# Kernel optimization log

Measured on AMD Instinct MI355X. Metric: run time of the kernel, lower is better.

The kernel has to match this reference:

```python
import jax, jax.numpy as jnp
import numpy as np

N, E = 20000, 640000
LATENT, HID, OUT, HEADS = 512, 256, 128, 2
NEG_SLOPE = 0.2


def setup_inputs() -> dict:
    key = jax.random.key(0)
    ks = jax.random.split(key, 12)
    s = 0.02
    return {
        "z": jax.random.normal(ks[0], (N, LATENT), dtype=jnp.float32),
        "edge_index": jax.random.randint(ks[1], (2, E), 0, N, dtype=jnp.int64),
        "W1": jax.random.normal(ks[2], (LATENT, HID), dtype=jnp.float32) * s,
        "b1": jnp.zeros((HID,), dtype=jnp.float32),
        "W2": jax.random.normal(ks[3], (HID, HID * HEADS), dtype=jnp.float32) * s,
        "b2": jnp.zeros((HID * HEADS,), dtype=jnp.float32),
        "Wg": jax.random.normal(ks[4], (HID * HEADS, HEADS * OUT), dtype=jnp.float32) * s,
        "att_src": jax.random.normal(ks[5], (HEADS, OUT), dtype=jnp.float32) * s,
        "att_dst": jax.random.normal(ks[6], (HEADS, OUT), dtype=jnp.float32) * s,
        "bias_g": jnp.zeros((HEADS * OUT,), dtype=jnp.float32),
        "W3": jax.random.normal(ks[7], (OUT * HEADS, 512), dtype=jnp.float32) * s,
        "b3": jnp.zeros((512,), dtype=jnp.float32),
    }


def _gat_conv(x, edge_index, Wg, att_src, att_dst, bias_g):
    n = x.shape[0]
    # add self loops (PyG GATConv default add_self_loops=True)
    loops = jnp.tile(jnp.arange(n, dtype=edge_index.dtype)[None, :], (2, 1))
    ei = jnp.concatenate([edge_index, loops], axis=1)
    src, dst = ei[0], ei[1]
    xp = (x @ Wg).reshape(n, HEADS, OUT)          # [N,H,C]
    a_src = jnp.einsum('nhc,hc->nh', xp, att_src)  # [N,H]
    a_dst = jnp.einsum('nhc,hc->nh', xp, att_dst)
    alpha = jax.nn.leaky_relu(a_src[src] + a_dst[dst], NEG_SLOPE)  # [E+N,H]
    amax = jax.ops.segment_max(alpha, dst, num_segments=n)
    alpha = jnp.exp(alpha - amax[dst])
    denom = jax.ops.segment_sum(alpha, dst, num_segments=n)
    alpha = alpha / jnp.maximum(denom[dst], 1e-16)
    msg = xp[src] * alpha[:, :, None]              # [E+N,H,C]
    out = jax.ops.segment_sum(msg, dst, num_segments=n)  # [N,H,C]
    return out.reshape(n, HEADS * OUT) + bias_g


def reference(z, edge_index, W1, b1, W2, b2, Wg, att_src, att_dst, bias_g, W3, b3):
    x = jax.nn.relu(z @ W1 + b1)
    x = jax.nn.relu(x @ W2 + b2)
    x = _gat_conv(x, edge_index, Wg, att_src, att_dst, bias_g)
    return x @ W3 + b3
```

## Files before the change

### kernel.cpp

```cpp
#include <hip/hip_runtime.h>
#include <hip/hip_bf16.h>
#include <float.h>

#define N_NODES 20000
#define LATENT  512
#define HID     256
#define OUT_C   128
#define HEADS   2
#define HC      256
#define NEG_SLOPE 0.2f

typedef _Float16 half8 __attribute__((ext_vector_type(8)));
typedef __attribute__((ext_vector_type(4))) float f32x4;
typedef __attribute__((ext_vector_type(2))) float f32x2;

__device__ __forceinline__ ushort f2h(float v) {
    _Float16 h = (_Float16)v;
    return *(ushort*)&h;
}
__device__ __forceinline__ float h2f(ushort u) {
    _Float16 h = *(_Float16*)&u;
    return (float)h;
}

#if __has_builtin(__builtin_amdgcn_cvt_pk_fp8_f32) && __has_builtin(__builtin_amdgcn_cvt_pk_f32_fp8)
#define FP8_HW 1
#else
#define FP8_HW 0
#endif

__device__ __forceinline__ uint f32_to_e4m3(float v) {
#if FP8_HW
    return (uint)(__builtin_amdgcn_cvt_pk_fp8_f32(v, v, 0, false) & 0xff);
#else
    _Float16 hf = (_Float16)(v * 0.00390625f);
    uint hb = *(ushort*)&hf;
    uint s = (hb >> 8) & 0x80;
    uint mag = hb & 0x7fff;
    mag = (mag + 0x3f + ((mag >> 7) & 1)) >> 7;
    if (mag > 0x7e) mag = 0x7e;
    return s | mag;
#endif
}

__device__ __forceinline__ void gl_lds16(const ushort* g, ushort* l) {
    __builtin_amdgcn_global_load_lds(
        (const __attribute__((address_space(1))) unsigned int*)g,
        (__attribute__((address_space(3))) unsigned int*)l, 16, 0, 0);
}

template<int BN, int LOGNBY>
__global__ __launch_bounds__(256, 4) void gemm_f16(
    const ushort* __restrict__ A, const ushort* __restrict__ BT,
    const float* __restrict__ bias,
    float* __restrict__ Cf, ushort* __restrict__ Ch,
    unsigned char* __restrict__ C8,
    const float* __restrict__ attS, const float* __restrict__ attD,
    float* __restrict__ aS, float* __restrict__ aD,
    int M, int N, int K, int relu)
{
    static_assert(BN == 64, "vmcnt immediates assume 3 DMAs/chunk");
    constexpr int NI  = BN / 32;
    constexpr int BUF = 4096 + BN * 32;
    __shared__ ushort lds[3 * BUF];

    const int t = threadIdx.x;
    const int l = t & 63;
    const int w = t >> 6;
    const int wm = (w >> 1) * 64;
    const int wn = (w & 1) * (BN / 2);
    const int lm = l & 15;
    const int q  = l >> 4;
    const int q4 = q * 4;

    const int T  = (int)gridDim.x;
    const int qq = T >> 3, rr = T & 7;
    const int kx = (int)blockIdx.x & 7;
    const int jx = (int)blockIdx.x >> 3;
    const int lin = kx * qq + (kx < rr ? kx : rr) + jx;
    const int row0 = (lin >> LOGNBY) * 128;
    const int col0 = (lin & ((1 << LOGNBY) - 1)) * BN;

    const int jr0 = w * 16 + (l >> 2);
    const int gsh = (((l & 3) ^ ((l >> 4) & 3)) << 3);
    const ushort* gA0 = A + (size_t)(row0 + jr0) * K + gsh;
    const ushort* gA1 = gA0 + (size_t)64 * K;
    const ushort* gB0 = BT + (size_t)(col0 + jr0) * K + gsh;
    const int dA0 = w * 512, dA1 = (4 + w) * 512;
    const int dB0 = 4096 + w * 512;

    const int csw = ((q ^ ((lm >> 2) & 3)) << 3);

    const f32x4 zf = {0.f, 0.f, 0.f, 0.f};
    f32x4 acc[4][NI];
    #pragma unroll
    for (int i = 0; i < 4; ++i)
        #pragma unroll
        for (int j = 0; j < NI; ++j) acc[i][j] = zf;

    const int NC = K >> 5;

    auto issue = [&](int c) {
        ushort* B = lds + (size_t)(c % 3) * BUF;
        const int kk = c * 32;
        gl_lds16(gA0 + kk, B + dA0);
        gl_lds16(gA1 + kk, B + dA1);
        gl_lds16(gB0 + kk, B + dB0);
    };

    auto compute = [&](int c) {
        const ushort* B = lds + (size_t)(c % 3) * BUF;
        half8 bf[NI];
        #pragma unroll
        for (int ni = 0; ni < NI; ++ni) {
            const int boff = (wn + ni * 16 + lm) * 32 + csw;
            bf[ni] = *(const half8*)&B[4096 + boff];
        }
        #pragma unroll
        for (int mi = 0; mi < 4; ++mi) {
            const int aoff = (wm + mi * 16 + lm) * 32 + csw;
            half8 af = *(const half8*)&B[aoff];
            #pragma unroll
            for (int ni = 0; ni < NI; ++ni)
                acc[mi][ni] = __builtin_amdgcn_mfma_f32_16x16x32_f16(
                    af, bf[ni], acc[mi][ni], 0, 0, 0);
        }
    };

    issue(0); issue(1);
    for (int c = 0; c < NC; ++c) {
        __builtin_amdgcn_sched_barrier(0);
        if (c + 1 < NC) asm volatile("s_waitcnt vmcnt(3)" ::: "memory");
        else            asm volatile("s_waitcnt vmcnt(0)" ::: "memory");
        __builtin_amdgcn_s_barrier();
        __builtin_amdgcn_sched_barrier(0);
        if (c + 2 < NC) issue(c + 2);
        compute(c);
    }

    #pragma unroll
    for (int mi = 0; mi < 4; ++mi) {
        #pragma unroll
        for (int ni = 0; ni < NI; ++ni) {
            const int col = col0 + wn + ni * 16 + lm;
            const float bv = bias ? bias[col] : 0.f;
            #pragma unroll
            for (int r = 0; r < 4; ++r) {
                const int row = row0 + wm + mi * 16 + q4 + r;
                if (row >= M) continue;
                float v = acc[mi][ni][r] + bv;
                if (relu) v = fmaxf(v, 0.f);
                const size_t idx = (size_t)row * N + col;
                if (Cf) Cf[idx] = v;
                if (Ch) Ch[idx] = f2h(v);
                if (C8) C8[idx] = (unsigned char)f32_to_e4m3(v);
            }
        }
    }

    if (aS) {
        const int h = (col0 >= OUT_C) ? 1 : 0;
        float asv[NI], adv[NI];
        #pragma unroll
        for (int ni = 0; ni < NI; ++ni) {
            const int c = col0 + wn + ni * 16 + lm;
            asv[ni] = attS[c];
            adv[ni] = attD[c];
        }
        #pragma unroll
        for (int mi = 0; mi < 4; ++mi) {
            #pragma unroll
            for (int r = 0; r < 4; ++r) {
                const int row = row0 + wm + mi * 16 + q4 + r;
                float ps = 0.f, pd = 0.f;
                #pragma unroll
                for (int ni = 0; ni < NI; ++ni) {
                    ps += acc[mi][ni][r] * asv[ni];
                    pd += acc[mi][ni][r] * adv[ni];
                }
                #pragma unroll
                for (int off = 8; off > 0; off >>= 1) {
                    ps += __shfl_xor(ps, off);
                    pd += __shfl_xor(pd, off);
                }
                if (lm == 0 && row < M) {
                    atomicAdd(&aS[2 * row + h], ps);
                    atomicAdd(&aD[2 * row + h], pd);
                }
            }
        }
    }
}

#define CVT_BLOCKS 10000
#define TR_BLOCKS  2048
__global__ __launch_bounds__(256) void prologue_kernel(
    const float* __restrict__ z, ushort* __restrict__ z_f16,
    int* deg, int* cursor, float* aS, float* aD, int n,
    const float* __restrict__ W1, const float* __restrict__ W2,
    const float* __restrict__ Wg, const float* __restrict__ W3,
    ushort* __restrict__ T1, ushort* __restrict__ T2,
    ushort* __restrict__ Tg, ushort* __restrict__ T3)
{
    const int b = blockIdx.x;
    if (b < CVT_BLOCKS) {
        int i = b * 256 + threadIdx.x;
        if (i < n) {
            deg[i] = 0; cursor[i] = 0;
            ((float2*)aS)[i] = make_float2(0.f, 0.f);
            ((float2*)aD)[i] = make_float2(0.f, 0.f);
        }
        float4 v = ((const float4*)z)[i];
        ((ushort4*)z_f16)[i] = make_ushort4(f2h(v.x), f2h(v.y), f2h(v.z), f2h(v.w));
    } else {
        int idx = (b - CVT_BLOCKS) * 256 + threadIdx.x;
        int which = idx >> 17, i = idx & 131071;
        const float* W; ushort* T; int K, N;
        if (which == 0)      { W = W1; T = T1; K = 512; N = 256; }
        else if (which == 1) { W = W2; T = T2; K = 256; N = 512; }
        else if (which == 2) { W = Wg; T = Tg; K = 512; N = 256; }
        else                 { W = W3; T = T3; K = 256; N = 512; }
        int k = i / N, nn = i - k * N;
        T[(size_t)nn * K + k] = f2h(W[i]);
    }
}

__global__ __launch_bounds__(256) void hist_kernel(
    const int* __restrict__ dst, int* deg, int E_real, int ET)
{
    int e = blockIdx.x * blockDim.x + threadIdx.x;
    if (e >= ET) return;
    int d = (e < E_real) ? dst[e] : (e - E_real);
    atomicAdd(&deg[d], 1);
}

__global__ __launch_bounds__(1024) void scan_kernel(
    const int* __restrict__ deg, int* __restrict__ rowptr, int n)
{
    __shared__ int part[1024];
    const int t = threadIdx.x;
    const int chunk = (n + 1023) / 1024;
    const int lo = t * chunk;
    const int hi = min(lo + chunk, n);
    int s = 0;
    for (int i = lo; i < hi; ++i) s += deg[i];
    part[t] = s;
    __syncthreads();
    #pragma unroll
    for (int off = 1; off < 1024; off <<= 1) {
        int add = (t >= off) ? part[t - off] : 0;
        __syncthreads();
        part[t] += add;
        __syncthreads();
    }
    int run = part[t] - s;
    for (int i = lo; i < hi; ++i) { rowptr[i] = run; run += deg[i]; }
    if (t == 1023) rowptr[n] = part[1023];
}

__global__ __launch_bounds__(256) void scatter_kernel(
    const int* __restrict__ src, const int* __restrict__ dst,
    const int* __restrict__ rowptr, int* cursor,
    int* __restrict__ sorted_src, int E_real, int ET)
{
    int e = blockIdx.x * blockDim.x + threadIdx.x;
    if (e >= ET) return;
    int s, d;
    if (e < E_real) { s = src[e]; d = dst[e]; }
    else            { s = e - E_real; d = s; }
    int pos = rowptr[d] + atomicAdd(&cursor[d], 1);
    sorted_src[pos] = s;
}

__global__ __launch_bounds__(256) void gat_aggregate(
    const int* __restrict__ rowptr, const int* __restrict__ sorted_src,
    const float* __restrict__ a_src, const float* __restrict__ a_dst,
    const unsigned char* __restrict__ xp8, const float* __restrict__ bias_g,
    ushort* __restrict__ xg, int n)
{
    const int d = blockIdx.x * 4 + (threadIdx.x >> 6);
    if (d >= n) return;
    const int lane = threadIdx.x & 63;
    const int hsel = lane & 32;
    const int start = rowptr[d], end = rowptr[d + 1];

    const float ad0 = a_dst[2 * d + 0];
    const float ad1 = a_dst[2 * d + 1];

    float4 acc = make_float4(0.f, 0.f, 0.f, 0.f);
    float denom = 0.f;

    for (int e0 = start; e0 < end; e0 += 32) {
        const int cnt = min(32, end - e0);
        const int idx = lane & 31;
        float wsel = 0.f; int off = 0;
        if (idx < cnt) {
            int s = sorted_src[e0 + idx];
            float v0 = a_src[2 * s + 0] + ad0;
            float v1 = a_src[2 * s + 1] + ad1;
            v0 = (v0 > 0.f) ? v0 : NEG_SLOPE * v0;
            v1 = (v1 > 0.f) ? v1 : NEG_SLOPE * v1;
            wsel = (lane < 32) ? __expf(v0) : __expf(v1);
            off = s * HC;
        }
        int j = 0;
        for (; j + 8 <= cnt; j += 8) {
            float w_[8]; int o_[8];
            #pragma unroll
            for (int u = 0; u < 8; ++u) {
                w_[u] = __shfl(wsel, (j + u) + hsel);
                o_[u] = __shfl(off, j + u);
            }
            uint v_[8];
            #pragma unroll
            for (int u = 0; u < 8; ++u)
                v_[u] = *(const uint*)(xp8 + o_[u] + 4 * lane);
            #pragma unroll
            for (int u = 0; u < 8; ++u) {
                denom += w_[u];
#if FP8_HW
                f32x2 lo = __builtin_amdgcn_cvt_pk_f32_fp8((int)v_[u], false);
                f32x2 hi = __builtin_amdgcn_cvt_pk_f32_fp8((int)v_[u], true);
                acc.x += w_[u] * lo.x; acc.y += w_[u] * lo.y;
                acc.z += w_[u] * hi.x; acc.w += w_[u] * hi.y;
#else
                const float wu = w_[u] * 256.0f;
                const uint b = v_[u];
                acc.x += wu * h2f(((b & 0x80u) << 8) | ((b & 0x7fu) << 7));
                acc.y += wu * h2f((((b >> 8) & 0x80u) << 8) | (((b >> 8) & 0x7fu) << 7));
                acc.z += wu * h2f((((b >> 16) & 0x80u) << 8) | (((b >> 16) & 0x7fu) << 7));
                acc.w += wu * h2f((((b >> 24) & 0x80u) << 8) | (((b >> 24) & 0x7fu) << 7));
#endif
            }
        }
        for (; j < cnt; ++j) {
            const float w = __shfl(wsel, j + hsel);
            const int   o = __shfl(off, j);
            const uint  b = *(const uint*)(xp8 + o + 4 * lane);
            denom += w;
#if FP8_HW
            f32x2 lo = __builtin_amdgcn_cvt_pk_f32_fp8((int)b, false);
            f32x2 hi = __builtin_amdgcn_cvt_pk_f32_fp8((int)b, true);
            acc.x += w * lo.x; acc.y += w * lo.y;
            acc.z += w * hi.x; acc.w += w * hi.y;
#else
            const float wu = w * 256.0f;
            acc.x += wu * h2f(((b & 0x80u) << 8) | ((b & 0x7fu) << 7));
            acc.y += wu * h2f((((b >> 8) & 0x80u) << 8) | (((b >> 8) & 0x7fu) << 7));
            acc.z += wu * h2f((((b >> 16) & 0x80u) << 8) | (((b >> 16) & 0x7fu) << 7));
            acc.w += wu * h2f((((b >> 24) & 0x80u) << 8) | (((b >> 24) & 0x7fu) << 7));
#endif
        }
    }

    const float inv = 1.f / fmaxf(denom, 1e-16f);
    const int c = 4 * lane;
    const float4 bg = *(const float4*)(bias_g + c);
    const size_t base = ((size_t)d * HC + c) >> 2;
    ((ushort4*)xg)[base] = make_ushort4(
        f2h(acc.x * inv + bg.x), f2h(acc.y * inv + bg.y),
        f2h(acc.z * inv + bg.z), f2h(acc.w * inv + bg.w));
}

extern "C" void kernel_launch(void* const* d_in, const int* in_sizes, int n_in,
                              void* d_out, int out_size, void* d_ws, size_t ws_size,
                              hipStream_t stream)
{
    const float* z       = (const float*)d_in[0];
    const int*   ei      = (const int*)d_in[1];
    const float* W1      = (const float*)d_in[2];
    const float* b1      = (const float*)d_in[3];
    const float* W2      = (const float*)d_in[4];
    const float* b2      = (const float*)d_in[5];
    const float* Wg      = (const float*)d_in[6];
    const float* att_src = (const float*)d_in[7];
    const float* att_dst = (const float*)d_in[8];
    const float* bias_g  = (const float*)d_in[9];
    const float* W3      = (const float*)d_in[10];
    const float* b3      = (const float*)d_in[11];
    float* out = (float*)d_out;

    const int n = N_NODES;
    const int E_real = in_sizes[1] / 2;
    const int ET = E_real + n;
    const int* src = ei;
    const int* dst = ei + E_real;

    char* p = (char*)d_ws;
    auto alloc = [&](size_t bytes) {
        char* r = p;
        p += (bytes + 63) & ~(size_t)63;
        return r;
    };
    const int np = n + 128;
    ushort* z_f16  = (ushort*)alloc((size_t)np * LATENT * 2);
    ushort* x1_f16 = (ushort*)alloc((size_t)np * HID * 2);
    unsigned char* xp8 = (unsigned char*)alloc((size_t)n * HC);
    ushort* W1T = (ushort*)alloc((size_t)LATENT * HID * 2);
    ushort* W2T = (ushort*)alloc((size_t)HID * 512 * 2);
    ushort* WgT = (ushort*)alloc((size_t)512 * HC * 2);
    ushort* W3T = (ushort*)alloc((size_t)HC * 512 * 2);
    float* a_src = (float*)alloc((size_t)2 * n * 4);
    float* a_dst = (float*)alloc((size_t)2 * n * 4);
    int* deg        = (int*)alloc((size_t)n * 4);
    int* rowptr     = (int*)alloc(((size_t)n + 1) * 4);
    int* cursor     = (int*)alloc((size_t)n * 4);
    int* sorted_src = (int*)alloc((size_t)ET * 4);
    ushort* x2_f16 = z_f16;
    ushort* xg_f16 = x1_f16;

    const int gm128 = (n + 127) / 128;

    prologue_kernel<<<CVT_BLOCKS + TR_BLOCKS, 256, 0, stream>>>(
        z, z_f16, deg, cursor, a_src, a_dst, n,
        W1, W2, Wg, W3, W1T, W2T, WgT, W3T);
    hist_kernel<<<(ET + 255) / 256, 256, 0, stream>>>(dst, deg, E_real, ET);
    scan_kernel<<<1, 1024, 0, stream>>>(deg, rowptr, n);
    scatter_kernel<<<(ET + 255) / 256, 256, 0, stream>>>(
        src, dst, rowptr, cursor, sorted_src, E_real, ET);

    gemm_f16<64, 2><<<gm128 * 4, 256, 0, stream>>>(
        z_f16, W1T, b1, nullptr, x1_f16, nullptr,
        nullptr, nullptr, nullptr, nullptr, n, HID, LATENT, 1);
    gemm_f16<64, 3><<<gm128 * 8, 256, 0, stream>>>(
        x1_f16, W2T, b2, nullptr, x2_f16, nullptr,
        nullptr, nullptr, nullptr, nullptr, n, 512, HID, 1);
    gemm_f16<64, 2><<<gm128 * 4, 256, 0, stream>>>(
        x2_f16, WgT, nullptr, nullptr, nullptr, xp8,
        att_src, att_dst, a_src, a_dst, n, HC, 512, 0);

    gat_aggregate<<<(n + 3) / 4, 256, 0, stream>>>(
        rowptr, sorted_src, a_src, a_dst, xp8, bias_g, xg_f16, n);

    gemm_f16<64, 3><<<gm128 * 8, 256, 0, stream>>>(
        xg_f16, W3T, b3, out, nullptr, nullptr,
        nullptr, nullptr, nullptr, nullptr, n, 512, HC, 0);
}
```

Baseline: 314.9 us.

## Fuse three MLP GEMMs into one kernel keeping intermediates in LDS

Replaces the three separate GEMM launches (W1, W2, Wg with attention-score epilogue) with a single 512-thread kernel. Each block handles 64 rows and keeps the x1 and x2 intermediates in LDS as swizzled f16, streaming weight chunks through a three-stage global-to-LDS buffer. This removes the HBM round trips for x1 and x2 and two launches. In exchange each block uses 128KB of LDS, so occupancy is one block per CU, and every block re-reads the full weight matrices.

New measurement: 296.5 us. 5.8% less time.

```diff
diff --git a/kernel.cpp b/kernel.cpp
--- a/kernel.cpp
+++ b/kernel.cpp
@@ -49,14 +49,217 @@
         (__attribute__((address_space(3))) unsigned int*)l, 16, 0, 0);
 }
 
+__global__ __launch_bounds__(512) void fused_mlp(
+    const ushort* __restrict__ z16, const ushort* __restrict__ W1T,
+    const float* __restrict__ b1, const ushort* __restrict__ W2T,
+    const float* __restrict__ b2, const ushort* __restrict__ WgT,
+    const float* __restrict__ attS, const float* __restrict__ attD,
+    float* __restrict__ aS, float* __restrict__ aD,
+    unsigned char* __restrict__ xp8, int M)
+{
+    __shared__ ushort lds[65536];
+
+    const int t = threadIdx.x;
+    const int l = t & 63;
+    const int w = t >> 6;
+    const int wr = w & 3;
+    const int wc = w >> 2;
+    const int lm = l & 15;
+    const int q  = l >> 4;
+    const int q4 = q * 4;
+    const int row0 = (int)blockIdx.x * 64;
+    const int lr16 = l >> 2;
+    const int gsh = (((l & 3) ^ ((l >> 4) & 3)) << 3);
+    const int csw = ((q ^ ((lm >> 2) & 3)) << 3);
+
+    constexpr int X1 = 0;
+    constexpr int X2 = 16384;
+    constexpr int SB = 49152;
+
+    auto p1b = [&](int c) { int b = c % 3; return b == 0 ? SB : b == 1 ? X2 : X2 + 10240; };
+    auto p2b = [&](int c) { int b = c % 3; return b == 0 ? SB : b == 1 ? X2 : X2 + 16384; };
+    auto p3b = [&](int c) { int b = c % 3; return b == 0 ? SB : b == 1 ? SB + 8192 : X1; };
+
+    auto issue1 = [&](int c) {
+        ushort* B = &lds[p1b(c)];
+        const int kk = c * 32;
+        #pragma unroll
+        for (int u = 0; u < 3; ++u) {
+            const int ii = w + u * 8;
+            if (ii < 20) {
+                const ushort* g = (ii < 4)
+                    ? z16 + (size_t)(row0 + ii * 16 + lr16) * 512 + kk + gsh
+                    : W1T + (size_t)((ii - 4) * 16 + lr16) * 512 + kk + gsh;
+                gl_lds16(g, B + ii * 512);
+            }
+        }
+    };
+    auto issue2 = [&](int c) {
+        ushort* B = &lds[p2b(c)];
+        const int kk = c * 32;
+        #pragma unroll
+        for (int u = 0; u < 4; ++u) {
+            const int ii = w + u * 8;
+            gl_lds16(W2T + (size_t)(ii * 16 + lr16) * 256 + kk + gsh, B + ii * 512);
+        }
+    };
+    auto issue3 = [&](int c) {
+        ushort* B = &lds[p3b(c)];
+        const int kk = c * 32;
+        #pragma unroll
+        for (int u = 0; u < 2; ++u) {
+            const int ii = w + u * 8;
+            gl_lds16(WgT + (size_t)(ii * 16 + lr16) * 512 + kk + gsh, B + ii * 512);
+        }
+    };
+
+    auto wait3i = [&](int c, int NC) {
+        __builtin_amdgcn_sched_barrier(0);
+        if (c + 1 < NC) {
+            if (w < 4) asm volatile("s_waitcnt vmcnt(3)" ::: "memory");
+            else       asm volatile("s_waitcnt vmcnt(2)" ::: "memory");
+        } else         asm volatile("s_waitcnt vmcnt(0)" ::: "memory");
+        __builtin_amdgcn_s_barrier();
+        __builtin_amdgcn_sched_barrier(0);
+    };
+    auto wait4 = [&](int c, int NC) {
+        __builtin_amdgcn_sched_barrier(0);
+        if (c + 1 < NC) asm volatile("s_waitcnt vmcnt(4)" ::: "memory");
+        else            asm volatile("s_waitcnt vmcnt(0)" ::: "memory");
+        __builtin_amdgcn_s_barrier();
+        __builtin_amdgcn_sched_barrier(0);
+    };
+    auto wait2 = [&](int c, int NC) {
+        __builtin_amdgcn_sched_barrier(0);
+        if (c + 1 < NC) asm volatile("s_waitcnt vmcnt(2)" ::: "memory");
+        else            asm volatile("s_waitcnt vmcnt(0)" ::: "memory");
+        __builtin_amdgcn_s_barrier();
+        __builtin_amdgcn_sched_barrier(0);
+    };
+
+    const f32x4 zf = {0.f, 0.f, 0.f, 0.f};
+
+    f32x4 acc1[8];
+    #pragma unroll
+    for (int i = 0; i < 8; ++i) acc1[i] = zf;
+
+    issue1(0); issue1(1);
+    for (int c = 0; c < 16; ++c) {
+        wait3i(c, 16);
+        if (c + 2 < 16) issue1(c + 2);
+        const ushort* B = &lds[p1b(c)];
+        half8 af = *(const half8*)&B[(wr * 16 + lm) * 32 + csw];
+        #pragma unroll
+        for (int ni = 0; ni < 8; ++ni) {
+            half8 bf = *(const half8*)&B[2048 + (wc * 128 + ni * 16 + lm) * 32 + csw];
+            acc1[ni] = __builtin_amdgcn_mfma_f32_16x16x32_f16(af, bf, acc1[ni], 0, 0, 0);
+        }
+    }
+    __builtin_amdgcn_s_barrier();
+    issue2(0); issue2(1);
+    #pragma unroll
+    for (int ni = 0; ni < 8; ++ni) {
+        const int col = wc * 128 + ni * 16 + lm;
+        const float bv = b1[col];
+        const int ch = col >> 5, c5 = col & 31;
+        #pragma unroll
+        for (int r = 0; r < 4; ++r) {
+            const int row = wr * 16 + q4 + r;
+            const float v = fmaxf(acc1[ni][r] + bv, 0.f);
+            lds[X1 + ch * 2048 + row * 32 + (((c5 >> 3) ^ q) << 3) + (c5 & 7)] = f2h(v);
+        }
+    }
+    asm volatile("s_waitcnt lgkmcnt(0)" ::: "memory");
+    __builtin_amdgcn_s_barrier();
+    __builtin_amdgcn_sched_barrier(0);
+
+    f32x4 acc2[16];
+    #pragma unroll
+    for (int i = 0; i < 16; ++i) acc2[i] = zf;
+
+    for (int c = 0; c < 8; ++c) {
+        wait4(c, 8);
+        if (c + 2 < 8) issue2(c + 2);
+        const ushort* B = &lds[p2b(c)];
+        half8 af = *(const half8*)&lds[X1 + c * 2048 + (wr * 16 + lm) * 32 + csw];
+        #pragma unroll
+        for (int ni = 0; ni < 16; ++ni) {
+            half8 bf = *(const half8*)&B[(wc * 256 + ni * 16 + lm) * 32 + csw];
+            acc2[ni] = __builtin_amdgcn_mfma_f32_16x16x32_f16(af, bf, acc2[ni], 0, 0, 0);
+        }
+    }
+    __builtin_amdgcn_s_barrier();
+    issue3(0); issue3(1);
+    #pragma unroll
+    for (int ni = 0; ni < 16; ++ni) {
+        const int col = wc * 256 + ni * 16 + lm;
+        const float bv = b2[col];
+        const int ch = col >> 5, c5 = col & 31;
+        #pragma unroll
+        for (int r = 0; r < 4; ++r) {
+            const int row = wr * 16 + q4 + r;
+            const float v = fmaxf(acc2[ni][r] + bv, 0.f);
+            lds[X2 + ch * 2048 + row * 32 + (((c5 >> 3) ^ q) << 3) + (c5 & 7)] = f2h(v);
+        }
+    }
+    asm volatile("s_waitcnt lgkmcnt(0)" ::: "memory");
+    __builtin_amdgcn_s_barrier();
+    __builtin_amdgcn_sched_barrier(0);
+
+    f32x4 acc3[8];
+    #pragma unroll
+    for (int i = 0; i < 8; ++i) acc3[i] = zf;
+
+    for (int c = 0; c < 16; ++c) {
+        wait2(c, 16);
+        if (c + 2 < 16) issue3(c + 2);
+        const ushort* B = &lds[p3b(c)];
+        half8 af = *(const half8*)&lds[X2 + c * 2048 + (wr * 16 + lm) * 32 + csw];
+        #pragma unroll
+        for (int ni = 0; ni < 8; ++ni) {
+            half8 bf = *(const half8*)&B[(wc * 128 + ni * 16 + lm) * 32 + csw];
+            acc3[ni] = __builtin_amdgcn_mfma_f32_16x16x32_f16(af, bf, acc3[ni], 0, 0, 0);
+        }
+    }
+
+    const int h = wc;
+    float asv[8], adv[8];
+    #pragma unroll
+    for (int ni = 0; ni < 8; ++ni) {
+        const int col = wc * 128 + ni * 16 + lm;
+        asv[ni] = attS[col];
+        adv[ni] = attD[col];
+    }
+    #pragma unroll
+    for (int r = 0; r < 4; ++r) {
+        const int row = row0 + wr * 16 + q4 + r;
+        float ps = 0.f, pd = 0.f;
+        #pragma unroll
+        for (int ni = 0; ni < 8; ++ni) {
+            const float v = acc3[ni][r];
+            ps += v * asv[ni];
+            pd += v * adv[ni];
+            if (row < M)
+                xp8[(size_t)row * HC + wc * 128 + ni * 16 + lm] =
+                    (unsigned char)f32_to_e4m3(v);
+        }
+        #pragma unroll
+        for (int off = 8; off > 0; off >>= 1) {
+            ps += __shfl_xor(ps, off);
+            pd += __shfl_xor(pd, off);
+        }
+        if (lm == 0 && row < M) {
+            atomicAdd(&aS[2 * row + h], ps);
+            atomicAdd(&aD[2 * row + h], pd);
+        }
+    }
+}
+
 template<int BN, int LOGNBY>
 __global__ __launch_bounds__(256, 4) void gemm_f16(
     const ushort* __restrict__ A, const ushort* __restrict__ BT,
     const float* __restrict__ bias,
     float* __restrict__ Cf, ushort* __restrict__ Ch,
-    unsigned char* __restrict__ C8,
-    const float* __restrict__ attS, const float* __restrict__ attD,
-    float* __restrict__ aS, float* __restrict__ aD,
     int M, int N, int K, int relu)
 {
     static_assert(BN == 64, "vmcnt immediates assume 3 DMAs/chunk");
@@ -153,40 +356,6 @@
                 const size_t idx = (size_t)row * N + col;
                 if (Cf) Cf[idx] = v;
                 if (Ch) Ch[idx] = f2h(v);
-                if (C8) C8[idx] = (unsigned char)f32_to_e4m3(v);
-            }
-        }
-    }
-
-    if (aS) {
-        const int h = (col0 >= OUT_C) ? 1 : 0;
-        float asv[NI], adv[NI];
-        #pragma unroll
-        for (int ni = 0; ni < NI; ++ni) {
-            const int c = col0 + wn + ni * 16 + lm;
-            asv[ni] = attS[c];
-            adv[ni] = attD[c];
-        }
-        #pragma unroll
-        for (int mi = 0; mi < 4; ++mi) {
-            #pragma unroll
-            for (int r = 0; r < 4; ++r) {
-                const int row = row0 + wm + mi * 16 + q4 + r;
-                float ps = 0.f, pd = 0.f;
-                #pragma unroll
-                for (int ni = 0; ni < NI; ++ni) {
-                    ps += acc[mi][ni][r] * asv[ni];
-                    pd += acc[mi][ni][r] * adv[ni];
-                }
-                #pragma unroll
-                for (int off = 8; off > 0; off >>= 1) {
-                    ps += __shfl_xor(ps, off);
-                    pd += __shfl_xor(pd, off);
-                }
-                if (lm == 0 && row < M) {
-                    atomicAdd(&aS[2 * row + h], ps);
-                    atomicAdd(&aD[2 * row + h], pd);
-                }
             }
         }
     }
@@ -394,7 +563,7 @@
     };
     const int np = n + 128;
     ushort* z_f16  = (ushort*)alloc((size_t)np * LATENT * 2);
-    ushort* x1_f16 = (ushort*)alloc((size_t)np * HID * 2);
+    ushort* xg_f16 = (ushort*)alloc((size_t)np * HID * 2);
     unsigned char* xp8 = (unsigned char*)alloc((size_t)n * HC);
     ushort* W1T = (ushort*)alloc((size_t)LATENT * HID * 2);
     ushort* W2T = (ushort*)alloc((size_t)HID * 512 * 2);
@@ -406,8 +575,6 @@
     int* rowptr     = (int*)alloc(((size_t)n + 1) * 4);
     int* cursor     = (int*)alloc((size_t)n * 4);
     int* sorted_src = (int*)alloc((size_t)ET * 4);
-    ushort* x2_f16 = z_f16;
-    ushort* xg_f16 = x1_f16;
 
     const int gm128 = (n + 127) / 128;
 
@@ -419,20 +586,13 @@
     scatter_kernel<<<(ET + 255) / 256, 256, 0, stream>>>(
         src, dst, rowptr, cursor, sorted_src, E_real, ET);
 
-    gemm_f16<64, 2><<<gm128 * 4, 256, 0, stream>>>(
-        z_f16, W1T, b1, nullptr, x1_f16, nullptr,
-        nullptr, nullptr, nullptr, nullptr, n, HID, LATENT, 1);
-    gemm_f16<64, 3><<<gm128 * 8, 256, 0, stream>>>(
-        x1_f16, W2T, b2, nullptr, x2_f16, nullptr,
-        nullptr, nullptr, nullptr, nullptr, n, 512, HID, 1);
-    gemm_f16<64, 2><<<gm128 * 4, 256, 0, stream>>>(
-        x2_f16, WgT, nullptr, nullptr, nullptr, xp8,
-        att_src, att_dst, a_src, a_dst, n, HC, 512, 0);
+    fused_mlp<<<(n + 63) / 64, 512, 0, stream>>>(
+        z_f16, W1T, b1, W2T, b2, WgT,
+        att_src, att_dst, a_src, a_dst, xp8, n);
 
     gat_aggregate<<<(n + 3) / 4, 256, 0, stream>>>(
         rowptr, sorted_src, a_src, a_dst, xp8, bias_g, xg_f16, n);
 
     gemm_f16<64, 3><<<gm128 * 8, 256, 0, stream>>>(
-        xg_f16, W3T, b3, out, nullptr, nullptr,
-        nullptr, nullptr, nullptr, nullptr, n, 512, HC, 0);
-}
+        xg_f16, W3T, b3, out, nullptr, n, 512, HC, 0);
+}
```
